# Performance work log

Hardware: AMD Instinct MI355X
Metric: run time of the kernel (lower is better)

The kernel has to match this reference:

```python
import jax, jax.numpy as jnp
import numpy as np
from jax import lax

L, B, D = 2048, 16, 1024

def setup_inputs() -> dict:
    key = jax.random.key(0)
    k1, k2, k3 = jax.random.split(key, 3)
    prev_layer = jax.random.normal(k1, (L, B, D), dtype=jnp.float32)
    hidden = jax.random.normal(k2, (B, D), dtype=jnp.float32)
    W = jax.random.normal(k3, (3 * D, D), dtype=jnp.float32) * (1.0 / np.sqrt(D))
    b = jnp.zeros((3 * D,), dtype=jnp.float32)
    return {"prev_layer": prev_layer, "hidden": hidden, "W": W, "b": b}

def reference(prev_layer, hidden, W, b):
    # prev_layer: [L, B, D], hidden: [B, D], W: [3D, D], b: [3D]
    d = hidden.shape[-1]
    # nn.Linear: y = x @ W.T + b  (dropout p=0 -> identity)
    preact = jnp.einsum('lbi,oi->lbo', prev_layer, W) + b  # [L, B, 3D]
    x_t = preact[..., :d]                                   # candidate
    gates = jax.nn.sigmoid(preact[..., d:])                 # [L, B, 2D]
    z = gates[..., :d]
    h_gate = gates[..., d:]

    def step(h, zx):
        zt, xt = zx
        s = (1.0 - zt) * h + zt * xt
        return s, s

    hidden_final, ss = lax.scan(step, hidden, (z, x_t))     # ss: [L, B, D]
    out = (1.0 - h_gate) * ss + h_gate * prev_layer         # highway (input_size==output_size)
    return out, hidden_final
```

## Files before the change

### kernel.cpp

```cpp
#include <hip/hip_runtime.h>
#include <cstdint>

#define L_DIM 2048
#define B_DIM 16
#define D_DIM 1024
#define M_DIM (L_DIM*B_DIM)
#define N_DIM (3*D_DIM)
#define K_DIM D_DIM
#define NCH   (B_DIM*D_DIM)
#define SEG   64
#define SEGLEN (L_DIM/SEG)
#define CG    (NCH/8)

typedef __bf16 bf16x8 __attribute__((ext_vector_type(8)));
typedef float f32x4 __attribute__((ext_vector_type(4)));

__device__ inline float bf2f(ushort u){ return __uint_as_float(((unsigned)u)<<16); }
__device__ inline ushort f2bf(float f){
  unsigned u = __float_as_uint(f);
  u += 0x7fffu + ((u>>16)&1u);
  return (ushort)(u>>16);
}

__global__ __launch_bounds__(256) void cvt8(const float* __restrict__ in,
                                            ushort* __restrict__ out, int n8){
  int t = blockIdx.x*256 + threadIdx.x;
  if (t >= n8) return;
  const float4* p = (const float4*)(in + (size_t)t*8);
  float4 a = p[0], b = p[1];
  ushort r[8] = {f2bf(a.x),f2bf(a.y),f2bf(a.z),f2bf(a.w),
                 f2bf(b.x),f2bf(b.y),f2bf(b.z),f2bf(b.w)};
  *(uint4*)(out + (size_t)t*8) = *(const uint4*)r;
}

__global__ __launch_bounds__(256) void gemm_sru(
    const ushort* __restrict__ A,
    const ushort* __restrict__ Bt,
    const float* __restrict__ bias,
    ushort* __restrict__ xbuf, ushort* __restrict__ zbuf, ushort* __restrict__ hbuf)
{
  __shared__ ushort As[128*32];
  __shared__ ushort Bs[128*32];
  const int tid  = threadIdx.x;
  const int lane = tid & 63, w = tid >> 6;
  const int wm = w >> 1, wn = w & 1;
  const int bnb = blockIdx.x % (N_DIM/128);
  const int bmb = blockIdx.x / (N_DIM/128);
  const int bm = bmb*128, bn = bnb*128;

  f32x4 acc[4][4];
  #pragma unroll
  for (int i=0;i<4;i++)
    #pragma unroll
    for (int j=0;j<4;j++) acc[i][j] = (f32x4){0.f,0.f,0.f,0.f};

  const int lrow = lane & 15, lk = (lane>>4)*8;

  for (int k0 = 0; k0 < K_DIM; k0 += 32) {
    #pragma unroll
    for (int q=0;q<2;q++){
      int c = (w*2+q)*64 + lane;
      int row = c >> 2, k8 = (c&3)*8;
      __builtin_amdgcn_global_load_lds(
        (const __attribute__((address_space(1))) void*)(A + (size_t)(bm+row)*K_DIM + k0 + k8),
        (__attribute__((address_space(3))) void*)(As + c*8), 16, 0, 0);
      __builtin_amdgcn_global_load_lds(
        (const __attribute__((address_space(1))) void*)(Bt + (size_t)(bn+row)*K_DIM + k0 + k8),
        (__attribute__((address_space(3))) void*)(Bs + c*8), 16, 0, 0);
    }
    __syncthreads();

    bf16x8 af[4], bf[4];
    #pragma unroll
    for (int i=0;i<4;i++) af[i] = *(const bf16x8*)(As + (wm*64 + i*16 + lrow)*32 + lk);
    #pragma unroll
    for (int j=0;j<4;j++) bf[j] = *(const bf16x8*)(Bs + (wn*64 + j*16 + lrow)*32 + lk);
    #pragma unroll
    for (int i=0;i<4;i++)
      #pragma unroll
      for (int j=0;j<4;j++)
        acc[i][j] = __builtin_amdgcn_mfma_f32_16x16x32_bf16(af[i], bf[j], acc[i][j], 0,0,0);
    __syncthreads();
  }

  const int region = bn >> 10;
  ushort* dst = region==0 ? xbuf : (region==1 ? zbuf : hbuf);
  #pragma unroll
  for (int j=0;j<4;j++){
    int o = bn + wn*64 + j*16 + lrow;
    float bv = bias[o];
    int colr = o & (D_DIM-1);
    #pragma unroll
    for (int i=0;i<4;i++){
      #pragma unroll
      for (int r=0;r<4;r++){
        int m = bm + wm*64 + i*16 + (lane>>4)*4 + r;
        float v = acc[i][j][r] + bv;
        if (region) v = 1.f/(1.f + __expf(-v));
        dst[(size_t)m*D_DIM + colr] = f2bf(v);
      }
    }
  }
}

__global__ __launch_bounds__(256) void scan_pass1(
    const ushort* __restrict__ z, const ushort* __restrict__ x,
    float* __restrict__ Aout, float* __restrict__ Bout)
{
  int t = blockIdx.x*256 + threadIdx.x;
  int cg = t & (CG-1), g = t >> 11;
  int c0 = cg*8;
  size_t base = (size_t)g*SEGLEN*NCH + c0;
  float A[8], Bc[8];
  #pragma unroll
  for (int j=0;j<8;j++){ A[j]=1.f; Bc[j]=0.f; }
  #pragma unroll 4
  for (int i=0;i<SEGLEN;i++){
    uint4 zv = *(const uint4*)(z + base + (size_t)i*NCH);
    uint4 xv = *(const uint4*)(x + base + (size_t)i*NCH);
    const ushort* zp = (const ushort*)&zv;
    const ushort* xp = (const ushort*)&xv;
    #pragma unroll
    for (int j=0;j<8;j++){
      float zf = bf2f(zp[j]);
      float a  = 1.f - zf;
      float b  = zf * bf2f(xp[j]);
      Bc[j] = a*Bc[j] + b;
      A[j]  = a*A[j];
    }
  }
  float* Ao = Aout + (size_t)g*NCH + c0;
  float* Bo = Bout + (size_t)g*NCH + c0;
  *(float4*)Ao     = make_float4(A[0],A[1],A[2],A[3]);
  *(float4*)(Ao+4) = make_float4(A[4],A[5],A[6],A[7]);
  *(float4*)Bo     = make_float4(Bc[0],Bc[1],Bc[2],Bc[3]);
  *(float4*)(Bo+4) = make_float4(Bc[4],Bc[5],Bc[6],Bc[7]);
}

__global__ __launch_bounds__(256) void scan_pass2(
    const float* __restrict__ A, const float* __restrict__ B,
    const float* __restrict__ h0, float* __restrict__ seg, float* __restrict__ hfin)
{
  int c = blockIdx.x*256 + threadIdx.x;
  float s = h0[c];
  #pragma unroll 8
  for (int g=0; g<SEG; g++){
    seg[(size_t)g*NCH + c] = s;
    s = A[(size_t)g*NCH + c]*s + B[(size_t)g*NCH + c];
  }
  hfin[c] = s;
}

__global__ __launch_bounds__(256) void scan_pass3(
    const ushort* __restrict__ z, const ushort* __restrict__ x, const ushort* __restrict__ hg,
    const float* __restrict__ prev, const float* __restrict__ seg,
    float* __restrict__ out)
{
  int t = blockIdx.x*256 + threadIdx.x;
  int cg = t & (CG-1), g = t >> 11;
  int c0 = cg*8;
  float s[8];
  *(float4*)s     = *(const float4*)(seg + (size_t)g*NCH + c0);
  *(float4*)(s+4) = *(const float4*)(seg + (size_t)g*NCH + c0 + 4);
  size_t base = (size_t)g*SEGLEN*NCH + c0;
  #pragma unroll 2
  for (int i=0;i<SEGLEN;i++){
    size_t idx = base + (size_t)i*NCH;
    uint4 zv = *(const uint4*)(z+idx);
    uint4 xv = *(const uint4*)(x+idx);
    uint4 hv = *(const uint4*)(hg+idx);
    float4 p0 = *(const float4*)(prev+idx);
    float4 p1 = *(const float4*)(prev+idx+4);
    const ushort* zp=(const ushort*)&zv;
    const ushort* xp=(const ushort*)&xv;
    const ushort* hp=(const ushort*)&hv;
    float pv[8] = {p0.x,p0.y,p0.z,p0.w,p1.x,p1.y,p1.z,p1.w};
    float o[8];
    #pragma unroll
    for (int j=0;j<8;j++){
      float zf = bf2f(zp[j]);
      s[j] += zf*(bf2f(xp[j]) - s[j]);
      float hf = bf2f(hp[j]);
      o[j] = s[j] + hf*(pv[j] - s[j]);
    }
    *(float4*)(out+idx)   = make_float4(o[0],o[1],o[2],o[3]);
    *(float4*)(out+idx+4) = make_float4(o[4],o[5],o[6],o[7]);
  }
}

extern "C" void kernel_launch(void* const* d_in, const int* in_sizes, int n_in,
                              void* d_out, int out_size, void* d_ws, size_t ws_size,
                              hipStream_t stream) {
  const float* prev = (const float*)d_in[0];
  const float* h0   = (const float*)d_in[1];
  const float* W    = (const float*)d_in[2];
  const float* bias = (const float*)d_in[3];
  float* out  = (float*)d_out;
  float* hfin = out + (size_t)M_DIM*D_DIM;

  char* ws = (char*)d_ws;
  ushort* Ab = (ushort*)ws;
  ushort* Wb = (ushort*)(ws + (size_t)M_DIM*K_DIM*2);
  ushort* xb = (ushort*)(ws + (size_t)M_DIM*K_DIM*2 + (size_t)N_DIM*K_DIM*2);
  ushort* zb = xb + (size_t)M_DIM*D_DIM;
  ushort* hb = zb + (size_t)M_DIM*D_DIM;
  float* Abuf = (float*)ws;
  float* Bbuf = Abuf + (size_t)SEG*NCH;
  float* segb = Bbuf + (size_t)SEG*NCH;

  cvt8<<<(M_DIM*K_DIM/8 + 255)/256, 256, 0, stream>>>(prev, Ab, M_DIM*K_DIM/8);
  cvt8<<<(N_DIM*K_DIM/8 + 255)/256, 256, 0, stream>>>(W,    Wb, N_DIM*K_DIM/8);
  gemm_sru<<<(M_DIM/128)*(N_DIM/128), 256, 0, stream>>>(Ab, Wb, bias, xb, zb, hb);
  scan_pass1<<<(CG*SEG)/256, 256, 0, stream>>>(zb, xb, Abuf, Bbuf);
  scan_pass2<<<NCH/256, 256, 0, stream>>>(Abuf, Bbuf, h0, segb, hfin);
  scan_pass3<<<(CG*SEG)/256, 256, 0, stream>>>(zb, xb, hb, prev, segb, out);
}
```

Before: 434.0 us.

## Rewrite GEMM with 256x256 tiles, 4-stage LDS pipeline, swizzle, and XOR layout

Replaces the single-buffered 128x128 GEMM with a 256x256 tile, 512 threads, and a 4-deep ring of LDS buffers filled ahead by direct global-to-LDS loads. The main loop is split into two MFMA halves separated by barriers, with raised wave priority and explicit vmcnt waits. It also adds an XOR swizzle on LDS columns to avoid bank conflicts and a block-index swizzle for L2 locality. The goal is to hide global load latency and raise MFMA utilisation, at the cost of more LDS (128KB), more registers, and fragile hand-tuned waitcnt logic.

```diff
diff --git a/kernel.cpp b/kernel.cpp
--- a/kernel.cpp
+++ b/kernel.cpp
@@ -12,6 +12,10 @@
 #define SEGLEN (L_DIM/SEG)
 #define CG    (NCH/8)
 
+#define BK 32
+#define NKT (K_DIM/BK)
+#define BUFB 32768
+
 typedef __bf16 bf16x8 __attribute__((ext_vector_type(8)));
 typedef float f32x4 __attribute__((ext_vector_type(4)));
 
@@ -33,69 +37,128 @@
   *(uint4*)(out + (size_t)t*8) = *(const uint4*)r;
 }
 
-__global__ __launch_bounds__(256) void gemm_sru(
-    const ushort* __restrict__ A,
-    const ushort* __restrict__ Bt,
+__global__ __launch_bounds__(512, 2) void gemm_sru(
+    const ushort* __restrict__ gA,
+    const ushort* __restrict__ gB,
     const float* __restrict__ bias,
     ushort* __restrict__ xbuf, ushort* __restrict__ zbuf, ushort* __restrict__ hbuf)
 {
-  __shared__ ushort As[128*32];
-  __shared__ ushort Bs[128*32];
+  __shared__ ushort lds[4*BUFB/2];
+  char* ldsb = (char*)lds;
+
   const int tid  = threadIdx.x;
   const int lane = tid & 63, w = tid >> 6;
-  const int wm = w >> 1, wn = w & 1;
-  const int bnb = blockIdx.x % (N_DIM/128);
-  const int bmb = blockIdx.x / (N_DIM/128);
-  const int bm = bmb*128, bn = bnb*128;
-
-  f32x4 acc[4][4];
+  const int wm = w >> 2, wn = w & 3;
+
+  const int bid = blockIdx.x;
+  const int swz = (bid & 7)*192 + (bid >> 3);
+  const int bmb = swz / (N_DIM/256), bnb = swz % (N_DIM/256);
+  const int bm = bmb*256, bn = bnb*256;
+
+  const int xr     = (lane>>1) & 3;
+  const int cxor16 = ((lane>>4) ^ xr) * 16;
+  const int arow   = wm*128 + (lane & 15);
+  const int brow   = wn*64  + (lane & 15);
+
+  const int srow0 = tid >> 2;
+  const int srow1 = 128 + (tid >> 2);
+  const int sc16p = (tid & 3) ^ ((tid >> 3) & 3);
+  const int cb0 = tid*16, cb1 = 8192 + tid*16;
+
+  f32x4 acc[8][4];
   #pragma unroll
-  for (int i=0;i<4;i++)
+  for (int i=0;i<8;i++)
     #pragma unroll
     for (int j=0;j<4;j++) acc[i][j] = (f32x4){0.f,0.f,0.f,0.f};
 
-  const int lrow = lane & 15, lk = (lane>>4)*8;
-
-  for (int k0 = 0; k0 < K_DIM; k0 += 32) {
-    #pragma unroll
-    for (int q=0;q<2;q++){
-      int c = (w*2+q)*64 + lane;
-      int row = c >> 2, k8 = (c&3)*8;
-      __builtin_amdgcn_global_load_lds(
-        (const __attribute__((address_space(1))) void*)(A + (size_t)(bm+row)*K_DIM + k0 + k8),
-        (__attribute__((address_space(3))) void*)(As + c*8), 16, 0, 0);
-      __builtin_amdgcn_global_load_lds(
-        (const __attribute__((address_space(1))) void*)(Bt + (size_t)(bn+row)*K_DIM + k0 + k8),
-        (__attribute__((address_space(3))) void*)(Bs + c*8), 16, 0, 0);
-    }
-    __syncthreads();
-
-    bf16x8 af[4], bf[4];
-    #pragma unroll
-    for (int i=0;i<4;i++) af[i] = *(const bf16x8*)(As + (wm*64 + i*16 + lrow)*32 + lk);
-    #pragma unroll
-    for (int j=0;j<4;j++) bf[j] = *(const bf16x8*)(Bs + (wn*64 + j*16 + lrow)*32 + lk);
-    #pragma unroll
-    for (int i=0;i<4;i++)
-      #pragma unroll
-      for (int j=0;j<4;j++)
-        acc[i][j] = __builtin_amdgcn_mfma_f32_16x16x32_bf16(af[i], bf[j], acc[i][j], 0,0,0);
-    __syncthreads();
+  auto stageA = [&](int t){
+    int k0 = t*BK;
+    char* dst = ldsb + (t&3)*BUFB;
+    __builtin_amdgcn_global_load_lds(
+      (const __attribute__((address_space(1))) void*)(gA + (size_t)(bm+srow0)*K_DIM + k0 + sc16p*8),
+      (__attribute__((address_space(3))) void*)(dst + cb0), 16, 0, 0);
+    __builtin_amdgcn_global_load_lds(
+      (const __attribute__((address_space(1))) void*)(gA + (size_t)(bm+srow1)*K_DIM + k0 + sc16p*8),
+      (__attribute__((address_space(3))) void*)(dst + cb1), 16, 0, 0);
+  };
+  auto stageB = [&](int t){
+    int k0 = t*BK;
+    char* dst = ldsb + (t&3)*BUFB + 16384;
+    __builtin_amdgcn_global_load_lds(
+      (const __attribute__((address_space(1))) void*)(gB + (size_t)(bn+srow0)*K_DIM + k0 + sc16p*8),
+      (__attribute__((address_space(3))) void*)(dst + cb0), 16, 0, 0);
+    __builtin_amdgcn_global_load_lds(
+      (const __attribute__((address_space(1))) void*)(gB + (size_t)(bn+srow1)*K_DIM + k0 + sc16p*8),
+      (__attribute__((address_space(3))) void*)(dst + cb1), 16, 0, 0);
+  };
+
+  stageA(0); stageB(0);
+  stageA(1); stageB(1);
+  stageA(2); stageB(2);
+  asm volatile("s_waitcnt vmcnt(8)" ::: "memory");
+  __builtin_amdgcn_s_barrier();
+  asm volatile("" ::: "memory");
+
+  for (int t = 0; t < NKT; ++t) {
+    const char* A_ = ldsb + (t&3)*BUFB;
+    const char* B_ = ldsb + (t&3)*BUFB + 16384;
+    const bool st = (t <= NKT-4);
+
+    bf16x8 af[8];
+    #pragma unroll
+    for (int mf=0; mf<8; ++mf)
+      af[mf] = *(const bf16x8*)(A_ + (arow + mf*16)*64 + cxor16);
+    bf16x8 bf0 = *(const bf16x8*)(B_ + (brow +  0)*64 + cxor16);
+    bf16x8 bf1 = *(const bf16x8*)(B_ + (brow + 16)*64 + cxor16);
+    if (st) stageA(t+3);
+    asm volatile("" ::: "memory");
+    __builtin_amdgcn_s_barrier();
+    asm volatile("" ::: "memory");
+    __builtin_amdgcn_s_setprio(1);
+    #pragma unroll
+    for (int mf=0; mf<8; ++mf) {
+      acc[mf][0] = __builtin_amdgcn_mfma_f32_16x16x32_bf16(af[mf], bf0, acc[mf][0], 0,0,0);
+      acc[mf][1] = __builtin_amdgcn_mfma_f32_16x16x32_bf16(af[mf], bf1, acc[mf][1], 0,0,0);
+    }
+    __builtin_amdgcn_s_setprio(0);
+    asm volatile("" ::: "memory");
+    __builtin_amdgcn_s_barrier();
+    asm volatile("" ::: "memory");
+
+    bf16x8 bf2 = *(const bf16x8*)(B_ + (brow + 32)*64 + cxor16);
+    bf16x8 bf3 = *(const bf16x8*)(B_ + (brow + 48)*64 + cxor16);
+    if (st) stageB(t+3);
+    if (t < NKT-3)       asm volatile("s_waitcnt vmcnt(8)" ::: "memory");
+    else if (t == NKT-3) asm volatile("s_waitcnt vmcnt(4)" ::: "memory");
+    else                 asm volatile("s_waitcnt vmcnt(0)" ::: "memory");
+    asm volatile("" ::: "memory");
+    __builtin_amdgcn_s_barrier();
+    asm volatile("" ::: "memory");
+    __builtin_amdgcn_s_setprio(1);
+    #pragma unroll
+    for (int mf=0; mf<8; ++mf) {
+      acc[mf][2] = __builtin_amdgcn_mfma_f32_16x16x32_bf16(af[mf], bf2, acc[mf][2], 0,0,0);
+      acc[mf][3] = __builtin_amdgcn_mfma_f32_16x16x32_bf16(af[mf], bf3, acc[mf][3], 0,0,0);
+    }
+    __builtin_amdgcn_s_setprio(0);
+    asm volatile("" ::: "memory");
+    __builtin_amdgcn_s_barrier();
+    asm volatile("" ::: "memory");
   }
 
   const int region = bn >> 10;
   ushort* dst = region==0 ? xbuf : (region==1 ? zbuf : hbuf);
   #pragma unroll
-  for (int j=0;j<4;j++){
-    int o = bn + wn*64 + j*16 + lrow;
+  for (int nf=0; nf<4; ++nf){
+    int o = bn + wn*64 + nf*16 + (lane & 15);
     float bv = bias[o];
     int colr = o & (D_DIM-1);
     #pragma unroll
-    for (int i=0;i<4;i++){
+    for (int mf=0; mf<8; ++mf){
       #pragma unroll
       for (int r=0;r<4;r++){
-        int m = bm + wm*64 + i*16 + (lane>>4)*4 + r;
-        float v = acc[i][j][r] + bv;
+        int m = bm + wm*128 + mf*16 + (lane>>4)*4 + r;
+        float v = acc[mf][nf][r] + bv;
         if (region) v = 1.f/(1.f + __expf(-v));
         dst[(size_t)m*D_DIM + colr] = f2bf(v);
       }
@@ -210,7 +273,7 @@
 
   cvt8<<<(M_DIM*K_DIM/8 + 255)/256, 256, 0, stream>>>(prev, Ab, M_DIM*K_DIM/8);
   cvt8<<<(N_DIM*K_DIM/8 + 255)/256, 256, 0, stream>>>(W,    Wb, N_DIM*K_DIM/8);
-  gemm_sru<<<(M_DIM/128)*(N_DIM/128), 256, 0, stream>>>(Ab, Wb, bias, xb, zb, hb);
+  gemm_sru<<<(M_DIM/256)*(N_DIM/256), 512, 0, stream>>>(Ab, Wb, bias, xb, zb, hb);
   scan_pass1<<<(CG*SEG)/256, 256, 0, stream>>>(zb, xb, Abuf, Bbuf);
   scan_pass2<<<NCH/256, 256, 0, stream>>>(Abuf, Bbuf, h0, segb, hfin);
   scan_pass3<<<(CG*SEG)/256, 256, 0, stream>>>(zb, xb, hb, prev, segb, out);
```

After: 422.4 us. -2.7%, faster.

## Rewrite GEMM with 256x256 tiles, double-buffered swizzled LDS and staged epilogue

Applied to the files above, without the earlier changes.

The bf16 GEMM moves from 128x128 tiles with BK=32 and single-buffered LDS to 256x256 tiles with BK=64 and 512 threads. K-tiles are double-buffered, with global-to-LDS loads issued in quarter stages that interleave with MFMA quadrants under explicit vmcnt waits and barriers. It adds an XOR swizzle to avoid LDS bank conflicts, a block-index swizzle for L2 locality, and an epilogue that stages bf16 results through LDS so global stores are coalesced 16-byte writes. The cost is 128KB of LDS per block, higher register pressure, and a more fragile hand-scheduled pipeline.

```diff
diff --git a/kernel.cpp b/kernel.cpp
--- a/kernel.cpp
+++ b/kernel.cpp
@@ -12,6 +12,10 @@
 #define SEGLEN (L_DIM/SEG)
 #define CG    (NCH/8)
 
+#define BK 64
+#define NKT (K_DIM/BK)
+#define BUF 65536
+
 typedef __bf16 bf16x8 __attribute__((ext_vector_type(8)));
 typedef float f32x4 __attribute__((ext_vector_type(4)));
 
@@ -33,74 +37,158 @@
   *(uint4*)(out + (size_t)t*8) = *(const uint4*)r;
 }
 
-__global__ __launch_bounds__(256) void gemm_sru(
-    const ushort* __restrict__ A,
-    const ushort* __restrict__ Bt,
+#define GLOAD(gp, lp) __builtin_amdgcn_global_load_lds( \
+    (const __attribute__((address_space(1))) void*)(gp), \
+    (__attribute__((address_space(3))) void*)(lp), 16, 0, 0)
+
+__global__ __launch_bounds__(512, 2) void gemm_sru(
+    const ushort* __restrict__ gA,
+    const ushort* __restrict__ gB,
     const float* __restrict__ bias,
     ushort* __restrict__ xbuf, ushort* __restrict__ zbuf, ushort* __restrict__ hbuf)
 {
-  __shared__ ushort As[128*32];
-  __shared__ ushort Bs[128*32];
+  __shared__ ulong2 lds_[2*BUF/16];
+  char* ldsb = (char*)lds_;
+
   const int tid  = threadIdx.x;
   const int lane = tid & 63, w = tid >> 6;
-  const int wm = w >> 1, wn = w & 1;
-  const int bnb = blockIdx.x % (N_DIM/128);
-  const int bmb = blockIdx.x / (N_DIM/128);
-  const int bm = bmb*128, bn = bnb*128;
-
-  f32x4 acc[4][4];
+  const int wr = (w>>2)*64;
+  const int wc = (w&3)*32;
+
+  const int bid = blockIdx.x;
+  const int swz = (bid & 7)*192 + (bid >> 3);
+  const int bm = (swz / (N_DIM/256))*256, bn = (swz % (N_DIM/256))*256;
+
+  const int l15 = lane & 15, l4 = lane >> 4, l7 = lane & 7;
+  const int s0 = ((l4)     ^ l7) * 16;
+  const int s1 = ((4 + l4) ^ l7) * 16;
+  const char* pA0 = ldsb + (wr + l15)*128 + s0;
+  const char* pA1 = ldsb + (wr + l15)*128 + s1;
+  const char* pB0 = ldsb + 32768 + (wc + l15)*128 + s0;
+  const char* pB1 = ldsb + 32768 + (wc + l15)*128 + s1;
+
+  const int gks = (tid & 7) ^ ((tid >> 3) & 7);
+  const size_t gArow = (size_t)(bm + (tid>>3))*K_DIM + gks*8;
+  const size_t gBrow = (size_t)(bn + (tid>>3))*K_DIM + gks*8;
+
+  f32x4 acc[4][8];
   #pragma unroll
   for (int i=0;i<4;i++)
     #pragma unroll
-    for (int j=0;j<4;j++) acc[i][j] = (f32x4){0.f,0.f,0.f,0.f};
-
-  const int lrow = lane & 15, lk = (lane>>4)*8;
-
-  for (int k0 = 0; k0 < K_DIM; k0 += 32) {
-    #pragma unroll
-    for (int q=0;q<2;q++){
-      int c = (w*2+q)*64 + lane;
-      int row = c >> 2, k8 = (c&3)*8;
-      __builtin_amdgcn_global_load_lds(
-        (const __attribute__((address_space(1))) void*)(A + (size_t)(bm+row)*K_DIM + k0 + k8),
-        (__attribute__((address_space(3))) void*)(As + c*8), 16, 0, 0);
-      __builtin_amdgcn_global_load_lds(
-        (const __attribute__((address_space(1))) void*)(Bt + (size_t)(bn+row)*K_DIM + k0 + k8),
-        (__attribute__((address_space(3))) void*)(Bs + c*8), 16, 0, 0);
-    }
-    __syncthreads();
-
-    bf16x8 af[4], bf[4];
-    #pragma unroll
-    for (int i=0;i<4;i++) af[i] = *(const bf16x8*)(As + (wm*64 + i*16 + lrow)*32 + lk);
-    #pragma unroll
-    for (int j=0;j<4;j++) bf[j] = *(const bf16x8*)(Bs + (wn*64 + j*16 + lrow)*32 + lk);
-    #pragma unroll
-    for (int i=0;i<4;i++)
-      #pragma unroll
-      for (int j=0;j<4;j++)
-        acc[i][j] = __builtin_amdgcn_mfma_f32_16x16x32_bf16(af[i], bf[j], acc[i][j], 0,0,0);
-    __syncthreads();
+    for (int j=0;j<8;j++) acc[i][j] = (f32x4){0.f,0.f,0.f,0.f};
+
+#define STAGE_A(h, tt) do{ \
+    const ushort* g = gA + gArow + (size_t)(h)*128*K_DIM + (tt)*BK; \
+    char* d = ldsb + ((tt)&1)*BUF + (h)*16384 + tid*16; \
+    GLOAD(g, d); GLOAD(g + (size_t)64*K_DIM, d + 8192); \
+  }while(0)
+#define STAGE_B(h, tt) do{ \
+    const ushort* g = gB + gBrow + (size_t)(h)*128*K_DIM + (tt)*BK; \
+    char* d = ldsb + ((tt)&1)*BUF + 32768 + (h)*16384 + tid*16; \
+    GLOAD(g, d); GLOAD(g + (size_t)64*K_DIM, d + 8192); \
+  }while(0)
+
+#define RD_A(dst, QA, bo) { _Pragma("unroll") \
+    for (int fr=0; fr<4; ++fr){ \
+      dst[fr][0] = *(const bf16x8*)(pA0 + (bo) + (QA)*16384 + fr*2048); \
+      dst[fr][1] = *(const bf16x8*)(pA1 + (bo) + (QA)*16384 + fr*2048); } }
+#define RD_B(QB, bo) { _Pragma("unroll") \
+    for (int fc=0; fc<2; ++fc){ \
+      b[fc][0] = *(const bf16x8*)(pB0 + (bo) + (QB)*16384 + fc*2048); \
+      b[fc][1] = *(const bf16x8*)(pB1 + (bo) + (QB)*16384 + fc*2048); } }
+#define MFMA_Q(qi, asrc) { \
+    __builtin_amdgcn_s_setprio(1); \
+    _Pragma("unroll") \
+    for (int fr=0; fr<4; ++fr) \
+      _Pragma("unroll") \
+      for (int fc=0; fc<2; ++fc){ \
+        acc[qi][fr*2+fc] = __builtin_amdgcn_mfma_f32_16x16x32_bf16(asrc[fr][0], b[fc][0], acc[qi][fr*2+fc], 0,0,0); \
+        acc[qi][fr*2+fc] = __builtin_amdgcn_mfma_f32_16x16x32_bf16(asrc[fr][1], b[fc][1], acc[qi][fr*2+fc], 0,0,0); } \
+    __builtin_amdgcn_s_setprio(0); }
+#define BAR() asm volatile("" ::: "memory"); __builtin_amdgcn_s_barrier(); asm volatile("" ::: "memory")
+#define VM(n) asm volatile("s_waitcnt vmcnt(" #n ")" ::: "memory")
+
+  bf16x8 a0[4][2], a1[4][2], b[2][2];
+
+  STAGE_A(0,0); STAGE_B(0,0); STAGE_A(1,0); STAGE_B(1,0);
+  VM(4); BAR();
+
+  for (int t = 0; t < NKT-1; ++t) {
+    const int bo = (t&1)*BUF;
+    RD_A(a0, 0, bo); RD_B(0, bo);
+    STAGE_A(0, t+1);
+    VM(4); BAR();
+    MFMA_Q(0, a0); BAR();
+    RD_A(a1, 1, bo);
+    STAGE_B(0, t+1);
+    VM(4); BAR();
+    MFMA_Q(2, a1); BAR();
+    RD_B(1, bo);
+    STAGE_A(1, t+1);
+    VM(6); BAR();
+    MFMA_Q(3, a1); BAR();
+    STAGE_B(1, t+1);
+    VM(4); BAR();
+    MFMA_Q(1, a0); BAR();
+  }
+  {
+    const int bo = ((NKT-1)&1)*BUF;
+    RD_A(a0, 0, bo); RD_B(0, bo);
+    VM(2); BAR();
+    MFMA_Q(0, a0); BAR();
+    RD_A(a1, 1, bo);
+    VM(0); BAR();
+    MFMA_Q(2, a1); BAR();
+    RD_B(1, bo);
+    BAR();
+    MFMA_Q(3, a1); BAR();
+    MFMA_Q(1, a0); BAR();
   }
 
   const int region = bn >> 10;
   ushort* dst = region==0 ? xbuf : (region==1 ? zbuf : hbuf);
-  #pragma unroll
-  for (int j=0;j<4;j++){
-    int o = bn + wn*64 + j*16 + lrow;
-    float bv = bias[o];
-    int colr = o & (D_DIM-1);
-    #pragma unroll
-    for (int i=0;i<4;i++){
+  ushort* lds16 = (ushort*)ldsb;
+  float bv[2][2];
+  #pragma unroll
+  for (int qb=0; qb<2; ++qb)
+    #pragma unroll
+    for (int fc=0; fc<2; ++fc)
+      bv[qb][fc] = bias[bn + qb*128 + wc + fc*16 + l15];
+
+  #pragma unroll
+  for (int qa=0; qa<2; ++qa)
+    #pragma unroll
+    for (int qb=0; qb<2; ++qb){
+      const int qi = qa*2+qb;
       #pragma unroll
-      for (int r=0;r<4;r++){
-        int m = bm + wm*64 + i*16 + (lane>>4)*4 + r;
-        float v = acc[i][j][r] + bv;
-        if (region) v = 1.f/(1.f + __expf(-v));
-        dst[(size_t)m*D_DIM + colr] = f2bf(v);
-      }
+      for (int fr=0; fr<4; ++fr)
+        #pragma unroll
+        for (int fc=0; fc<2; ++fc)
+          #pragma unroll
+          for (int r=0; r<4; ++r){
+            int row = qa*128 + wr + fr*16 + l4*4 + r;
+            int col = qb*128 + wc + fc*16 + l15;
+            float v = acc[qi][fr*2+fc][r] + bv[qb][fc];
+            if (region) v = 1.f/(1.f + __expf(-v));
+            lds16[row*256 + col] = f2bf(v);
+          }
     }
-  }
+  __syncthreads();
+  const int cb = bn & (D_DIM-1);
+  #pragma unroll
+  for (int i=0;i<16;i++){
+    int off = i*8192 + tid*16;
+    int row = off >> 9;
+    int cols = (off & 511) >> 1;
+    *(uint4*)(dst + (size_t)(bm+row)*D_DIM + cb + cols) = *(const uint4*)(ldsb + off);
+  }
+#undef STAGE_A
+#undef STAGE_B
+#undef RD_A
+#undef RD_B
+#undef MFMA_Q
+#undef BAR
+#undef VM
 }
 
 __global__ __launch_bounds__(256) void scan_pass1(
@@ -124,8 +212,8 @@
     for (int j=0;j<8;j++){
       float zf = bf2f(zp[j]);
       float a  = 1.f - zf;
-      float b  = zf * bf2f(xp[j]);
-      Bc[j] = a*Bc[j] + b;
+      float bb = zf * bf2f(xp[j]);
+      Bc[j] = a*Bc[j] + bb;
       A[j]  = a*A[j];
     }
   }
@@ -210,7 +298,7 @@
 
   cvt8<<<(M_DIM*K_DIM/8 + 255)/256, 256, 0, stream>>>(prev, Ab, M_DIM*K_DIM/8);
   cvt8<<<(N_DIM*K_DIM/8 + 255)/256, 256, 0, stream>>>(W,    Wb, N_DIM*K_DIM/8);
-  gemm_sru<<<(M_DIM/128)*(N_DIM/128), 256, 0, stream>>>(Ab, Wb, bias, xb, zb, hb);
+  gemm_sru<<<(M_DIM/256)*(N_DIM/256), 512, 0, stream>>>(Ab, Wb, bias, xb, zb, hb);
   scan_pass1<<<(CG*SEG)/256, 256, 0, stream>>>(zb, xb, Abuf, Bbuf);
   scan_pass2<<<NCH/256, 256, 0, stream>>>(Abuf, Bbuf, h0, segb, hfin);
   scan_pass3<<<(CG*SEG)/256, 256, 0, stream>>>(zb, xb, hb, prev, segb, out);
```

Result: faster. 382.0 us (-12.0%).

## Restructure GEMM with 128x256 tiles, double-buffered LDS, swizzles and staged epilogue

Applied to the files above, without the earlier changes.

The GEMM kernel now uses 512-thread blocks computing 128x256 tiles, with double-buffered LDS so the next K-tile's global-to-LDS loads overlap the current tile's MFMAs. It also adds XOR swizzles on the LDS layout to reduce bank conflicts, block-index swizzling for L2 locality, and s_setprio around the MFMA groups. The epilogue stages bf16 results through LDS so global stores become coalesced 16-byte writes instead of scattered 2-byte ones. In exchange it relies on hand-placed waitcnt and barriers, which could introduce races, and it uses more registers per thread.

```diff
diff --git a/kernel.cpp b/kernel.cpp
--- a/kernel.cpp
+++ b/kernel.cpp
@@ -12,6 +12,14 @@
 #define SEGLEN (L_DIM/SEG)
 #define CG    (NCH/8)
 
+#define BM 128
+#define BN 256
+#define BK 32
+#define NKT (K_DIM/BK)
+#define ABY (BM*BK*2)
+#define BBY (BN*BK*2)
+#define BUFB (ABY+BBY)
+
 typedef __bf16 bf16x8 __attribute__((ext_vector_type(8)));
 typedef float f32x4 __attribute__((ext_vector_type(4)));
 
@@ -33,20 +41,36 @@
   *(uint4*)(out + (size_t)t*8) = *(const uint4*)r;
 }
 
-__global__ __launch_bounds__(256) void gemm_sru(
-    const ushort* __restrict__ A,
-    const ushort* __restrict__ Bt,
+#define GLOAD(gp, lp) __builtin_amdgcn_global_load_lds( \
+    (const __attribute__((address_space(1))) void*)(gp), \
+    (__attribute__((address_space(3))) void*)(lp), 16, 0, 0)
+
+__global__ __launch_bounds__(512, 4) void gemm_sru(
+    const ushort* __restrict__ gA,
+    const ushort* __restrict__ gB,
     const float* __restrict__ bias,
     ushort* __restrict__ xbuf, ushort* __restrict__ zbuf, ushort* __restrict__ hbuf)
 {
-  __shared__ ushort As[128*32];
-  __shared__ ushort Bs[128*32];
+  __shared__ ulong2 lds_[2*BUFB/16];
+  char* ldsb = (char*)lds_;
+
   const int tid  = threadIdx.x;
   const int lane = tid & 63, w = tid >> 6;
-  const int wm = w >> 1, wn = w & 1;
-  const int bnb = blockIdx.x % (N_DIM/128);
-  const int bmb = blockIdx.x / (N_DIM/128);
-  const int bm = bmb*128, bn = bnb*128;
+  const int wm = w >> 2, wn = w & 3;
+  const int l15 = lane & 15, l4 = lane >> 4;
+
+  const int bid = blockIdx.x;
+  const int swz = (bid & 7)*384 + (bid >> 3);
+  const int bnb = swz >> 8, bmb = swz & 255;
+  const int bm = bmb*BM, bn = bnb*BN;
+
+  const int offX = l15*64 + (((l4) ^ (lane&3))*16);
+  const int offA = wm*4096 + offX;
+  const int offB = ABY + wn*4096 + offX;
+
+  const int gsl = (tid & 3) ^ ((tid >> 2) & 3);
+  const ushort* gAp = gA + (size_t)(bm + (tid>>2))*K_DIM + gsl*8;
+  const ushort* gBp = gB + (size_t)(bn + (tid>>2))*K_DIM + gsl*8;
 
   f32x4 acc[4][4];
   #pragma unroll
@@ -54,53 +78,83 @@
     #pragma unroll
     for (int j=0;j<4;j++) acc[i][j] = (f32x4){0.f,0.f,0.f,0.f};
 
-  const int lrow = lane & 15, lk = (lane>>4)*8;
-
-  for (int k0 = 0; k0 < K_DIM; k0 += 32) {
-    #pragma unroll
-    for (int q=0;q<2;q++){
-      int c = (w*2+q)*64 + lane;
-      int row = c >> 2, k8 = (c&3)*8;
-      __builtin_amdgcn_global_load_lds(
-        (const __attribute__((address_space(1))) void*)(A + (size_t)(bm+row)*K_DIM + k0 + k8),
-        (__attribute__((address_space(3))) void*)(As + c*8), 16, 0, 0);
-      __builtin_amdgcn_global_load_lds(
-        (const __attribute__((address_space(1))) void*)(Bt + (size_t)(bn+row)*K_DIM + k0 + k8),
-        (__attribute__((address_space(3))) void*)(Bs + c*8), 16, 0, 0);
-    }
-    __syncthreads();
-
-    bf16x8 af[4], bf[4];
-    #pragma unroll
-    for (int i=0;i<4;i++) af[i] = *(const bf16x8*)(As + (wm*64 + i*16 + lrow)*32 + lk);
-    #pragma unroll
-    for (int j=0;j<4;j++) bf[j] = *(const bf16x8*)(Bs + (wn*64 + j*16 + lrow)*32 + lk);
-    #pragma unroll
-    for (int i=0;i<4;i++)
-      #pragma unroll
-      for (int j=0;j<4;j++)
-        acc[i][j] = __builtin_amdgcn_mfma_f32_16x16x32_bf16(af[i], bf[j], acc[i][j], 0,0,0);
-    __syncthreads();
+#define STAGE_A(tt) do{ \
+    GLOAD(gAp + (tt)*BK, ldsb + ((tt)&1)*BUFB + tid*16); \
+  }while(0)
+#define STAGE_B(tt) do{ \
+    GLOAD(gBp + (tt)*BK,                     ldsb + ((tt)&1)*BUFB + ABY + tid*16); \
+    GLOAD(gBp + (size_t)128*K_DIM + (tt)*BK, ldsb + ((tt)&1)*BUFB + ABY + 8192 + tid*16); \
+  }while(0)
+#define BAR() asm volatile("" ::: "memory"); __builtin_amdgcn_s_barrier(); asm volatile("" ::: "memory")
+#define VM(n) asm volatile("s_waitcnt vmcnt(" #n ")" ::: "memory")
+
+  STAGE_A(0); STAGE_B(0);
+  VM(0); BAR();
+
+  for (int t = 0; t < NKT; ++t) {
+    const int bo = (t&1)*BUFB;
+    bf16x8 af0 = *(const bf16x8*)(ldsb + bo + offA);
+    bf16x8 af1 = *(const bf16x8*)(ldsb + bo + offA + 1024);
+    bf16x8 af2 = *(const bf16x8*)(ldsb + bo + offA + 2048);
+    bf16x8 af3 = *(const bf16x8*)(ldsb + bo + offA + 3072);
+    if (t < NKT-1) { STAGE_A(t+1); VM(1); }
+    else           { VM(0); }
+    BAR();
+    #pragma unroll
+    for (int nt=0; nt<4; ++nt) {
+      bf16x8 bfv = *(const bf16x8*)(ldsb + bo + offB + nt*1024);
+      __builtin_amdgcn_s_setprio(1);
+      acc[0][nt] = __builtin_amdgcn_mfma_f32_16x16x32_bf16(af0, bfv, acc[0][nt], 0,0,0);
+      acc[1][nt] = __builtin_amdgcn_mfma_f32_16x16x32_bf16(af1, bfv, acc[1][nt], 0,0,0);
+      acc[2][nt] = __builtin_amdgcn_mfma_f32_16x16x32_bf16(af2, bfv, acc[2][nt], 0,0,0);
+      acc[3][nt] = __builtin_amdgcn_mfma_f32_16x16x32_bf16(af3, bfv, acc[3][nt], 0,0,0);
+      __builtin_amdgcn_s_setprio(0);
+    }
+    if (t < NKT-1) { STAGE_B(t+1); VM(2); }
+    BAR();
   }
 
   const int region = bn >> 10;
   ushort* dst = region==0 ? xbuf : (region==1 ? zbuf : hbuf);
-  #pragma unroll
-  for (int j=0;j<4;j++){
-    int o = bn + wn*64 + j*16 + lrow;
-    float bv = bias[o];
-    int colr = o & (D_DIM-1);
-    #pragma unroll
-    for (int i=0;i<4;i++){
+  const int cb = bn & (D_DIM-1);
+  ushort* lds16 = (ushort*)ldsb;
+  float bv[4];
+  #pragma unroll
+  for (int nt=0; nt<4; ++nt) bv[nt] = bias[bn + wn*64 + nt*16 + l15];
+
+  #pragma unroll
+  for (int h=0; h<2; ++h) {
+    if (wm == h) {
       #pragma unroll
-      for (int r=0;r<4;r++){
-        int m = bm + wm*64 + i*16 + (lane>>4)*4 + r;
-        float v = acc[i][j][r] + bv;
-        if (region) v = 1.f/(1.f + __expf(-v));
-        dst[(size_t)m*D_DIM + colr] = f2bf(v);
-      }
-    }
-  }
+      for (int mt=0; mt<4; ++mt)
+        #pragma unroll
+        for (int nt=0; nt<4; ++nt)
+          #pragma unroll
+          for (int r=0; r<4; ++r) {
+            int lrow = mt*16 + l4*4 + r;
+            int col  = wn*64 + nt*16 + l15;
+            float v = acc[mt][nt][r] + bv[nt];
+            if (region) v = 1.f/(1.f + __expf(-v));
+            int slot = col >> 3;
+            lds16[lrow*256 + (((slot ^ (lrow&31))&31)<<3) + (col&7)] = f2bf(v);
+          }
+    }
+    __syncthreads();
+    #pragma unroll
+    for (int i=0; i<4; ++i) {
+      int off = i*8192 + tid*16;
+      int lrow = off >> 9;
+      int slot = (off >> 4) & 31;
+      int dcol = (off & 511) >> 1;
+      const char* src = ldsb + lrow*512 + (((slot ^ (lrow&31))&31)<<4);
+      *(uint4*)(dst + (size_t)(bm + h*64 + lrow)*D_DIM + cb + dcol) = *(const uint4*)src;
+    }
+    __syncthreads();
+  }
+#undef STAGE_A
+#undef STAGE_B
+#undef BAR
+#undef VM
 }
 
 __global__ __launch_bounds__(256) void scan_pass1(
@@ -124,8 +178,8 @@
     for (int j=0;j<8;j++){
       float zf = bf2f(zp[j]);
       float a  = 1.f - zf;
-      float b  = zf * bf2f(xp[j]);
-      Bc[j] = a*Bc[j] + b;
+      float bb = zf * bf2f(xp[j]);
+      Bc[j] = a*Bc[j] + bb;
       A[j]  = a*A[j];
     }
   }
@@ -210,7 +264,7 @@
 
   cvt8<<<(M_DIM*K_DIM/8 + 255)/256, 256, 0, stream>>>(prev, Ab, M_DIM*K_DIM/8);
   cvt8<<<(N_DIM*K_DIM/8 + 255)/256, 256, 0, stream>>>(W,    Wb, N_DIM*K_DIM/8);
-  gemm_sru<<<(M_DIM/128)*(N_DIM/128), 256, 0, stream>>>(Ab, Wb, bias, xb, zb, hb);
+  gemm_sru<<<(M_DIM/BM)*(N_DIM/BN), 512, 0, stream>>>(Ab, Wb, bias, xb, zb, hb);
   scan_pass1<<<(CG*SEG)/256, 256, 0, stream>>>(zb, xb, Abuf, Bbuf);
   scan_pass2<<<NCH/256, 256, 0, stream>>>(Abuf, Bbuf, h0, segb, hfin);
   scan_pass3<<<(CG*SEG)/256, 256, 0, stream>>>(zb, xb, hb, prev, segb, out);
```

After: 402.3 us. 1.08x faster.
